# Kernel tuning notes

Measured on AMD Instinct MI355X. Metric: run time of the kernel, lower is better.

The kernel has to match this reference:

```python
import jax, jax.numpy as jnp
import numpy as np

B, N = 256, 8192
H = 30
NUM_CLASSES = 5


def setup_inputs() -> dict:
    key = jax.random.key(0)
    ks = jax.random.split(key, 16)
    def dense(k, fi, fo):
        # flax default: lecun_normal kernel, zero bias
        return jax.random.normal(k, (fi, fo), jnp.float32) / jnp.sqrt(fi)
    return {
        'x':   jax.random.normal(ks[0], (B, N), jnp.float32),
        'W1':  dense(ks[1], 1, H),   'b1': jnp.zeros((H,), jnp.float32),
        'W2':  dense(ks[2], H, H),   'b2': jnp.zeros((H,), jnp.float32),
        'Wa1': dense(ks[3], H, 32),  'ba1': jnp.zeros((32,), jnp.float32),
        'Wa2': dense(ks[4], 32, 1),  'ba2': jnp.zeros((1,), jnp.float32),
        'Wf1': dense(ks[5], 6 * H, 40), 'bf1': jnp.zeros((40,), jnp.float32),
        'Wf2': dense(ks[6], 40, 40),    'bf2': jnp.zeros((40,), jnp.float32),
        'Wf3': dense(ks[7], 40, NUM_CLASSES), 'bf3': jnp.zeros((NUM_CLASSES,), jnp.float32),
    }


def reference(x, W1, b1, W2, b2, Wa1, ba1, Wa2, ba2, Wf1, bf1, Wf2, bf2, Wf3, bf3):
    # (B, N) -> (B, N, 1) -> Dense(30) -> relu -> Dense(30)
    h = jax.nn.relu(x[..., None] * W1[0] + b1)          # (B, N, 30)
    h = jnp.einsum('bnh,hk->bnk', h, W2) + b2           # (B, N, 30)

    # statistical pools over the point axis (axis=1)
    mean_pool = jnp.mean(h, axis=1)
    max_pool = jnp.max(h, axis=1)
    min_pool = jnp.min(h, axis=1)
    std_pool = jnp.std(h, axis=1)
    sum_pool = jnp.sum(h, axis=1)

    # attention pooling over points
    a = jax.nn.relu(jnp.einsum('bnh,hk->bnk', h, Wa1) + ba1)  # (B, N, 32)
    logits = jnp.einsum('bnk,ko->bno', a, Wa2) + ba2          # (B, N, 1)
    attn = jax.nn.softmax(logits, axis=1)                     # (B, N, 1)
    attention_pool = jnp.sum(h * attn, axis=1)                # (B, 30)

    feat = jnp.concatenate(
        [mean_pool, max_pool, min_pool, std_pool, sum_pool, attention_pool],
        axis=-1)                                              # (B, 180)

    z = jax.nn.relu(feat @ Wf1 + bf1)
    z = jax.nn.relu(z @ Wf2 + bf2)
    return z @ Wf3 + bf3                                      # (B, num_classes)
```

## Files before the change

### kernel.cpp

```cpp
#include <hip/hip_runtime.h>
#include <math.h>

#define NN 8192
#define HH 30
#define TPB 1024
#define NIV 31
#define TSTR 68

__launch_bounds__(TPB)
__global__ void pointnet_pwl7_kernel(
    const float* __restrict__ x,
    const float* __restrict__ W1,  const float* __restrict__ b1,
    const float* __restrict__ W2,  const float* __restrict__ b2,
    const float* __restrict__ Wa1, const float* __restrict__ ba1,
    const float* __restrict__ Wa2, const float* __restrict__ ba2,
    const float* __restrict__ Wf1, const float* __restrict__ bf1,
    const float* __restrict__ Wf2, const float* __restrict__ bf2,
    const float* __restrict__ Wf3, const float* __restrict__ bf3,
    float* __restrict__ out)
{
    __shared__ float W2s[HH][32];
    __shared__ float Wa1s[HH][32];
    __shared__ float P[HH][32];
    __shared__ float w1s[HH], b1s[HH], tts[HH];
    __shared__ float b2s[32], ba1s[32], Wa2s[32], vb2[32];
    __shared__ int   DcS;
    __shared__ float d0S;
    __shared__ __align__(16) float ab2[2][64];
    __shared__ __align__(16) float uv2[2][64];
    __shared__ float zz_raw[128], zz_s[128];
    __shared__ float2 gcs[129];
    __shared__ __align__(16) float ts_s[32];
    __shared__ int   rnk[HH];
    __shared__ __align__(16) float abt[NIV][TSTR];
    __shared__ __align__(16) float uvt[NIV][TSTR];
    __shared__ float redb[16][155];
    __shared__ float fin[16];
    __shared__ float feat[192];
    __shared__ float redh[12][40];
    __shared__ float z1s[40], z2s[40];
    __shared__ float wf1s[180 * 40];
    __shared__ float wf2s[40 * 40];
    __shared__ float wf3s[40 * 5];
    __shared__ float bf1s[40], bf2s[40], bf3s[8];

    const int tid = threadIdx.x;
    const int b   = blockIdx.x;

    float4 xl0, xl1;
    {
        const float4* xb4 = reinterpret_cast<const float4*>(x + (size_t)b * NN);
        xl0 = xb4[tid];
        xl1 = xb4[tid + TPB];
    }

    for (int i = tid; i < HH * 32; i += TPB) {
        int j = i >> 5, k = i & 31;
        W2s[j][k] = (k < HH) ? W2[j * HH + k] : 0.f;
    }
    for (int i = tid; i < HH * 32; i += TPB) ((float*)Wa1s)[i] = Wa1[i];
    for (int i = tid; i < 180 * 40; i += TPB) wf1s[i] = Wf1[i];
    for (int i = tid; i < 40 * 40;  i += TPB) wf2s[i] = Wf2[i];
    if (tid < 40 * 5) wf3s[tid] = Wf3[tid];
    if (tid < HH) {
        float w = W1[tid], bb = b1[tid];
        w1s[tid] = w; b1s[tid] = bb;
        tts[tid] = (w != 0.f) ? (-bb / w) : INFINITY;
    }
    if (tid < 32) {
        b2s[tid]  = (tid < HH) ? b2[tid] : 0.f;
        ba1s[tid] = ba1[tid];
        Wa2s[tid] = Wa2[tid];
        ts_s[tid] = INFINITY;
    }
    if (tid < 40) { bf1s[tid] = bf1[tid]; bf2s[tid] = bf2[tid]; }
    if (tid < 5)  { bf3s[tid] = bf3[tid]; }
    const float ba2v = ba2[0];
    __syncthreads();

    if (tid < HH * 32) {
        int j = tid >> 5, m = tid & 31;
        float s = 0.f;
        #pragma unroll
        for (int k = 0; k < HH; ++k) s = fmaf(W2s[j][k], Wa1s[k][m], s);
        P[j][m] = s;
    } else if (tid < HH * 32 + 32) {
        int m = tid - HH * 32;
        float s = 0.f;
        #pragma unroll
        for (int k = 0; k < HH; ++k) s = fmaf(Wa1s[k][m], b2s[k], s);
        vb2[m] = s;
    }
    if (tid < 64) {
        float t = (tid < HH) ? tts[tid] : INFINITY;
        bool fin_t = (t < INFINITY);
        float tmin = fin_t ? t :  INFINITY;
        float tmax = fin_t ? t : -INFINITY;
        #pragma unroll
        for (int off = 32; off > 0; off >>= 1) {
            tmin = fminf(tmin, __shfl_xor(tmin, off));
            tmax = fmaxf(tmax, __shfl_xor(tmax, off));
        }
        if (tid == 0) {
            bool dc1 = (tmin < INFINITY) && (tmin == tmax);
            DcS = dc1 ? 1 : 0;
            d0S = tmin;
        }
    }
    __syncthreads();

    if (DcS == 1) {
        const float d0 = d0S;

        if (tid < 64) {
            int r = tid >> 5, k = tid & 31;
            float a = 0.f, bb = 0.f;
            if (k < HH) {
                for (int j = 0; j < HH; ++j) {
                    float w = w1s[j];
                    bool act = (w == 0.f) ? (b1s[j] > 0.f) : (r ? (w > 0.f) : (w < 0.f));
                    if (act) {
                        float w2 = W2s[j][k];
                        a  = fmaf(w,      w2, a);
                        bb = fmaf(b1s[j], w2, bb);
                    }
                }
                bb += b2s[k];
            }
            ab2[r][k]      = a;
            ab2[r][32 + k] = bb;
        } else if (tid < 128) {
            int i2 = tid - 64;
            int r = i2 >> 5, m = i2 & 31;
            float u = 0.f, v = 0.f;
            for (int j = 0; j < HH; ++j) {
                float w = w1s[j];
                bool act = (w == 0.f) ? (b1s[j] > 0.f) : (r ? (w > 0.f) : (w < 0.f));
                if (act) {
                    float pj = P[j][m];
                    u = fmaf(w,      pj, u);
                    v = fmaf(b1s[j], pj, v);
                }
            }
            v += vb2[m] + ba1s[m];
            uv2[r][m]      = u;
            uv2[r][32 + m] = v;
            float zr = -v / u;
            bool ok = (u != 0.f) && (r == 0 ? (zr < d0) : (zr > d0));
            zz_raw[1 + i2] = ok ? zr : INFINITY;
        } else if (tid < 191) {
            zz_raw[tid - 63] = INFINITY;
        } else if (tid == 191) {
            zz_raw[0] = d0;
        }
        __syncthreads();

        if (tid < 128) {
            float v = zz_raw[tid];
            int rk = 0;
            for (int i = 0; i < 128; ++i) {
                float vi = zz_raw[i];
                rk += (vi < v) || (vi == v && i < tid);
            }
            zz_s[rk] = v;
        }
        __syncthreads();

        if (tid < 129) {
            float lo = (tid == 0)   ? -INFINITY : zz_s[tid - 1];
            float hi = (tid == 128) ?  INFINITY : zz_s[tid];
            float xm;
            if (lo == -INFINITY)      xm = (hi < INFINITY) ? hi - 1.f : 0.f;
            else if (hi == INFINITY)  xm = lo + 1.f;
            else                      xm = 0.5f * (lo + hi);
            int r = (xm >= d0) ? 1 : 0;
            float g = 0.f, c = ba2v;
            for (int m = 0; m < 32; ++m) {
                float u = uv2[r][m], v = uv2[r][32 + m];
                if (fmaf(u, xm, v) > 0.f) {
                    float w = Wa2s[m];
                    g = fmaf(w, u, g);
                    c = fmaf(w, v, c);
                }
            }
            gcs[tid] = make_float2(g, c);
        }
        __syncthreads();

        float c0=0,c1=0, Sx0=0,Sx1=0, Q0=0,Q1=0;
        float mn0=INFINITY,mn1=INFINITY, mx0=-INFINITY,mx1=-INFINITY;
        float Sp0=0,Sp1=0, Px0=0,Px1=0;
        float mrun = -INFINITY;

        float xs[8] = {xl0.x, xl0.y, xl0.z, xl0.w, xl1.x, xl1.y, xl1.z, xl1.w};
        #pragma unroll
        for (int pp = 0; pp < 8; ++pp) {
            float xv = xs[pp];
            bool q1 = (xv >= d0);
            int idx = 0;
            #pragma unroll
            for (int bit = 64; bit >= 1; bit >>= 1) {
                int t = idx + bit;
                idx = (zz_s[t - 1] <= xv) ? t : idx;
            }
            float2 gc = gcs[idx];
            float l = fmaf(xv, gc.x, gc.y);
            float dlt = l - mrun, p;
            if (dlt > 8.f) {
                float sc = __expf(-dlt);
                Sp0 *= sc; Sp1 *= sc; Px0 *= sc; Px1 *= sc;
                mrun = l; p = 1.f;
            } else p = __expf(dlt);
            float xx = xv * xv, px = p * xv;
            float i1 = q1 ? 1.f : 0.f, i0 = 1.f - i1;
            c0 += i0;                    c1 += i1;
            Sx0 = fmaf(i0, xv, Sx0);     Sx1 = fmaf(i1, xv, Sx1);
            Q0  = fmaf(i0, xx, Q0);      Q1  = fmaf(i1, xx, Q1);
            Sp0 = fmaf(i0, p,  Sp0);     Sp1 = fmaf(i1, p,  Sp1);
            Px0 = fmaf(i0, px, Px0);     Px1 = fmaf(i1, px, Px1);
            mn0 = fminf(mn0, q1 ?  INFINITY : xv);
            mx0 = fmaxf(mx0, q1 ? -INFINITY : xv);
            mn1 = fminf(mn1, q1 ? xv :  INFINITY);
            mx1 = fmaxf(mx1, q1 ? xv : -INFINITY);
        }

        #pragma unroll 1
        for (int off = 32; off > 0; off >>= 1) {
            c0  += __shfl_xor(c0,  off);  c1  += __shfl_xor(c1,  off);
            Sx0 += __shfl_xor(Sx0, off);  Sx1 += __shfl_xor(Sx1, off);
            Q0  += __shfl_xor(Q0,  off);  Q1  += __shfl_xor(Q1,  off);
            mn0 = fminf(mn0, __shfl_xor(mn0, off));
            mn1 = fminf(mn1, __shfl_xor(mn1, off));
            mx0 = fmaxf(mx0, __shfl_xor(mx0, off));
            mx1 = fmaxf(mx1, __shfl_xor(mx1, off));
            float mo = __shfl_xor(mrun, off);
            float M  = fmaxf(mrun, mo);
            float sa = __expf(mrun - M), sb = __expf(mo - M);
            float t;
            t = __shfl_xor(Sp0, off); Sp0 = Sp0 * sa + t * sb;
            t = __shfl_xor(Sp1, off); Sp1 = Sp1 * sa + t * sb;
            t = __shfl_xor(Px0, off); Px0 = Px0 * sa + t * sb;
            t = __shfl_xor(Px1, off); Px1 = Px1 * sa + t * sb;
            mrun = M;
        }

        const int wave = tid >> 6, lane = tid & 63;
        if (lane == 0) {
            float* rw = redb[wave];
            rw[0]=c0; rw[1]=Sx0; rw[2]=Q0; rw[3]=mn0; rw[4]=mx0; rw[5]=Sp0; rw[6]=Px0;
            rw[7]=c1; rw[8]=Sx1; rw[9]=Q1; rw[10]=mn1; rw[11]=mx1; rw[12]=Sp1; rw[13]=Px1;
            rw[14]=mrun;
        }
        __syncthreads();

        if (tid < 2) {
            float M = redb[0][14];
            #pragma unroll
            for (int w = 1; w < 16; ++w) M = fmaxf(M, redb[w][14]);
            int base = tid * 7;
            float ck=0, Sx=0, Q=0, mnv=INFINITY, mxv=-INFINITY, Sp=0, Px=0;
            #pragma unroll
            for (int w = 0; w < 16; ++w) {
                ck += redb[w][base+0]; Sx += redb[w][base+1]; Q += redb[w][base+2];
                mnv = fminf(mnv, redb[w][base+3]); mxv = fmaxf(mxv, redb[w][base+4]);
                float e = __expf(redb[w][14] - M);
                Sp = fmaf(redb[w][base+5], e, Sp);
                Px = fmaf(redb[w][base+6], e, Px);
            }
            fin[base+0]=ck; fin[base+1]=Sx; fin[base+2]=Q;
            fin[base+3]=mnv; fin[base+4]=mxv; fin[base+5]=Sp; fin[base+6]=Px;
        }
        __syncthreads();

        if (tid < HH) {
            float sumk=0, ssqk=0, acck=0, L=0;
            float mxk=-INFINITY, mnk=INFINITY;
            #pragma unroll
            for (int r2 = 0; r2 < 2; ++r2) {
                float ck = fin[r2*7+0], Sx = fin[r2*7+1], Q = fin[r2*7+2];
                float xmn = fin[r2*7+3], xmx = fin[r2*7+4];
                float Sp = fin[r2*7+5], Px = fin[r2*7+6];
                float a = ab2[r2][tid], bb = ab2[r2][32 + tid];
                sumk += a * Sx + bb * ck;
                ssqk += a * a * Q + 2.f * a * bb * Sx + bb * bb * ck;
                acck += a * Px + bb * Sp;
                L += Sp;
                if (ck > 0.f) {
                    float h1 = fmaf(a, xmn, bb), h2v = fmaf(a, xmx, bb);
                    mxk = fmaxf(mxk, fmaxf(h1, h2v));
                    mnk = fminf(mnk, fminf(h1, h2v));
                }
            }
            const float invN = 1.f / (float)NN;
            float mean = sumk * invN;
            float var  = fmaxf(ssqk * invN - mean * mean, 0.f);
            feat[tid]        = mean;
            feat[30 + tid]   = mxk;
            feat[60 + tid]   = mnk;
            feat[90 + tid]   = sqrtf(var);
            feat[120 + tid]  = sumk;
            feat[150 + tid]  = acck / L;
        }
    } else {
        if (tid < HH) {
            float t = tts[tid];
            int r = 0;
            for (int i = 0; i < HH; ++i) {
                float ti = tts[i];
                r += (ti < t) || (ti == t && i < tid);
            }
            ts_s[r] = t;
            rnk[tid] = r;
        }
        __syncthreads();
        for (int idx = tid; idx < NIV * 32; idx += TPB) {
            int r = idx >> 5, k = idx & 31;
            float a = 0.f, bb = 0.f;
            if (k < HH) {
                for (int j = 0; j < HH; ++j) {
                    float w = w1s[j];
                    bool act = (w > 0.f) ? (rnk[j] < r)
                             : ((w < 0.f) ? (rnk[j] >= r) : (b1s[j] > 0.f));
                    if (act) {
                        float w2 = W2s[j][k];
                        a  = fmaf(w,      w2, a);
                        bb = fmaf(b1s[j], w2, bb);
                    }
                }
                bb += b2s[k];
            }
            abt[r][k]      = a;
            abt[r][32 + k] = bb;
        }
        __syncthreads();
        for (int idx = tid; idx < NIV * 32; idx += TPB) {
            int r = idx >> 5, m = idx & 31;
            float u = 0.f, v = 0.f;
            for (int k = 0; k < HH; ++k) {
                float wa = Wa1s[k][m];
                u = fmaf(wa, abt[r][k],      u);
                v = fmaf(wa, abt[r][32 + k], v);
            }
            v += ba1s[m];
            uvt[r][m]      = u;
            uvt[r][32 + m] = v;
        }
        __syncthreads();

        float sum[HH], ssq[HH], mx[HH], mn[HH], acc[HH];
        #pragma unroll
        for (int k = 0; k < HH; ++k) {
            sum[k] = 0.f; ssq[k] = 0.f; acc[k] = 0.f;
            mx[k] = -INFINITY; mn[k] = INFINITY;
        }
        float mrun = -INFINITY, lrun = 0.f;
        const float* xb = x + (size_t)b * NN;
        const float4* ts4 = (const float4*)ts_s;
        const float4* wv4 = (const float4*)Wa2s;

        #pragma unroll 1
        for (int it = 0; it < NN / TPB; ++it) {
            float xv = xb[it * TPB + tid];
            int r = 0;
            #pragma unroll
            for (int i = 0; i < 8; ++i) {
                float4 t = ts4[i];
                r += (xv >= t.x) ? 1 : 0;
                r += (xv >= t.y) ? 1 : 0;
                r += (xv >= t.z) ? 1 : 0;
                r += (xv >= t.w) ? 1 : 0;
            }
            float h2[HH];
            const float4* arow = (const float4*)(&abt[r][0]);
            #pragma unroll
            for (int i = 0; i < 7; ++i) {
                float4 av = arow[i], bv = arow[8 + i];
                h2[4*i+0] = fmaf(xv, av.x, bv.x);
                h2[4*i+1] = fmaf(xv, av.y, bv.y);
                h2[4*i+2] = fmaf(xv, av.z, bv.z);
                h2[4*i+3] = fmaf(xv, av.w, bv.w);
            }
            { float4 av = arow[7], bv = arow[15];
              h2[28] = fmaf(xv, av.x, bv.x);
              h2[29] = fmaf(xv, av.y, bv.y); }
            #pragma unroll
            for (int k = 0; k < HH; ++k) {
                float h = h2[k];
                sum[k] += h;
                ssq[k] = fmaf(h, h, ssq[k]);
                mx[k] = fmaxf(mx[k], h);
                mn[k] = fminf(mn[k], h);
            }
            float l = ba2v;
            const float4* urow = (const float4*)(&uvt[r][0]);
            #pragma unroll
            for (int i = 0; i < 8; ++i) {
                float4 uu = urow[i], vv = urow[8 + i], ww = wv4[i];
                l = fmaf(fmaxf(fmaf(xv, uu.x, vv.x), 0.f), ww.x, l);
                l = fmaf(fmaxf(fmaf(xv, uu.y, vv.y), 0.f), ww.y, l);
                l = fmaf(fmaxf(fmaf(xv, uu.z, vv.z), 0.f), ww.z, l);
                l = fmaf(fmaxf(fmaf(xv, uu.w, vv.w), 0.f), ww.w, l);
            }
            float d = l - mrun, p;
            if (d > 8.f) {
                float s = __expf(-d);
                lrun *= s;
                #pragma unroll
                for (int k = 0; k < HH; ++k) acc[k] *= s;
                mrun = l; p = 1.f;
            } else p = __expf(d);
            lrun += p;
            #pragma unroll
            for (int k = 0; k < HH; ++k) acc[k] = fmaf(p, h2[k], acc[k]);
        }

        #pragma unroll 1
        for (int off = 32; off > 0; off >>= 1) {
            #pragma unroll
            for (int k = 0; k < HH; ++k) {
                sum[k] += __shfl_xor(sum[k], off);
                ssq[k] += __shfl_xor(ssq[k], off);
                mx[k] = fmaxf(mx[k], __shfl_xor(mx[k], off));
                mn[k] = fminf(mn[k], __shfl_xor(mn[k], off));
            }
            float mo = __shfl_xor(mrun, off);
            float lo = __shfl_xor(lrun, off);
            float M  = fmaxf(mrun, mo);
            float sa = __expf(mrun - M), sb = __expf(mo - M);
            lrun = lrun * sa + lo * sb;
            #pragma unroll
            for (int k = 0; k < HH; ++k)
                acc[k] = acc[k] * sa + __shfl_xor(acc[k], off) * sb;
            mrun = M;
        }

        const int wave = tid >> 6, lane = tid & 63;
        if (lane == 0) {
            #pragma unroll
            for (int k = 0; k < HH; ++k) {
                redb[wave][k]       = sum[k];
                redb[wave][30 + k]  = ssq[k];
                redb[wave][60 + k]  = mx[k];
                redb[wave][90 + k]  = mn[k];
                redb[wave][120 + k] = acc[k];
            }
            redb[wave][150] = mrun;
            redb[wave][151] = lrun;
        }
        __syncthreads();

        if (tid < HH) {
            float M = -INFINITY;
            #pragma unroll
            for (int w = 0; w < 16; ++w) M = fmaxf(M, redb[w][150]);
            float s = 0.f, ss = 0.f, L = 0.f, A = 0.f;
            float mxv = -INFINITY, mnv = INFINITY;
            #pragma unroll
            for (int w = 0; w < 16; ++w) {
                s  += redb[w][tid];
                ss += redb[w][30 + tid];
                mxv = fmaxf(mxv, redb[w][60 + tid]);
                mnv = fminf(mnv, redb[w][90 + tid]);
                float e = __expf(redb[w][150] - M);
                L = fmaf(redb[w][151], e, L);
                A = fmaf(redb[w][120 + tid], e, A);
            }
            const float invN = 1.f / (float)NN;
            float mean = s * invN;
            float var  = fmaxf(ss * invN - mean * mean, 0.f);
            feat[tid]       = mean;
            feat[30 + tid]  = mxv;
            feat[60 + tid]  = mnv;
            feat[90 + tid]  = sqrtf(var);
            feat[120 + tid] = s;
            feat[150 + tid] = A / L;
        }
    }
    __syncthreads();

    if (tid < 480) {
        int o = tid % 40, p = tid / 40;
        float z = 0.f;
        #pragma unroll
        for (int ii = 0; ii < 15; ++ii)
            z = fmaf(feat[p * 15 + ii], wf1s[(p * 15 + ii) * 40 + o], z);
        redh[p][o] = z;
    }
    __syncthreads();
    if (tid < 40) {
        float z = bf1s[tid];
        #pragma unroll
        for (int p = 0; p < 12; ++p) z += redh[p][tid];
        z1s[tid] = fmaxf(z, 0.f);
    }
    __syncthreads();
    if (tid < 40) {
        float z = bf2s[tid];
        #pragma unroll
        for (int i = 0; i < 40; ++i) z = fmaf(z1s[i], wf2s[i * 40 + tid], z);
        z2s[tid] = fmaxf(z, 0.f);
    }
    __syncthreads();
    if (tid < 5) {
        float o = bf3s[tid];
        #pragma unroll
        for (int i = 0; i < 40; ++i) o = fmaf(z2s[i], wf3s[i * 5 + tid], o);
        out[b * 5 + tid] = o;
    }
}

extern "C" void kernel_launch(void* const* d_in, const int* in_sizes, int n_in,
                              void* d_out, int out_size, void* d_ws, size_t ws_size,
                              hipStream_t stream) {
    const float* x   = (const float*)d_in[0];
    const float* W1  = (const float*)d_in[1];
    const float* b1  = (const float*)d_in[2];
    const float* W2  = (const float*)d_in[3];
    const float* b2  = (const float*)d_in[4];
    const float* Wa1 = (const float*)d_in[5];
    const float* ba1 = (const float*)d_in[6];
    const float* Wa2 = (const float*)d_in[7];
    const float* ba2 = (const float*)d_in[8];
    const float* Wf1 = (const float*)d_in[9];
    const float* bf1 = (const float*)d_in[10];
    const float* Wf2 = (const float*)d_in[11];
    const float* bf2 = (const float*)d_in[12];
    const float* Wf3 = (const float*)d_in[13];
    const float* bf3 = (const float*)d_in[14];
    float* out = (float*)d_out;

    pointnet_pwl7_kernel<<<256, TPB, 0, stream>>>(
        x, W1, b1, W2, b2, Wa1, ba1, Wa2, ba2,
        Wf1, bf1, Wf2, bf2, Wf3, bf3, out);
}
```

Measured before the change: 113.6 us.

## Split fast and fallback paths into separate kernels gated by workspace flag

The single kernel held both the fast piecewise-linear path (used when all first-layer ReLU breakpoints coincide) and the general fallback, so its shared memory and register footprint were sized for the fallback. The fast path now lives in its own 1024-thread kernel with a smaller reduction buffer, and writes a flag to workspace. A second 512-thread fallback kernel reads the flag and exits immediately when the fast path already ran. This is meant to lower resource pressure on the fast path, at the cost of an extra kernel launch and a flag read.

```diff
diff --git a/kernel.cpp b/kernel.cpp
--- a/kernel.cpp
+++ b/kernel.cpp
@@ -3,12 +3,13 @@
 
 #define NN 8192
 #define HH 30
-#define TPB 1024
+#define TPBA 1024
+#define TPBB 512
 #define NIV 31
 #define TSTR 68
 
-__launch_bounds__(TPB)
-__global__ void pointnet_pwl7_kernel(
+__launch_bounds__(TPBA)
+__global__ void pointnet_fastA(
     const float* __restrict__ x,
     const float* __restrict__ W1,  const float* __restrict__ b1,
     const float* __restrict__ W2,  const float* __restrict__ b2,
@@ -17,7 +18,7 @@
     const float* __restrict__ Wf1, const float* __restrict__ bf1,
     const float* __restrict__ Wf2, const float* __restrict__ bf2,
     const float* __restrict__ Wf3, const float* __restrict__ bf3,
-    float* __restrict__ out)
+    float* __restrict__ out, int* __restrict__ wsflag)
 {
     __shared__ float W2s[HH][32];
     __shared__ float Wa1s[HH][32];
@@ -30,11 +31,7 @@
     __shared__ __align__(16) float uv2[2][64];
     __shared__ float zz_raw[128], zz_s[128];
     __shared__ float2 gcs[129];
-    __shared__ __align__(16) float ts_s[32];
-    __shared__ int   rnk[HH];
-    __shared__ __align__(16) float abt[NIV][TSTR];
-    __shared__ __align__(16) float uvt[NIV][TSTR];
-    __shared__ float redb[16][155];
+    __shared__ float redb[16][16];
     __shared__ float fin[16];
     __shared__ float feat[192];
     __shared__ float redh[12][40];
@@ -51,16 +48,16 @@
     {
         const float4* xb4 = reinterpret_cast<const float4*>(x + (size_t)b * NN);
         xl0 = xb4[tid];
-        xl1 = xb4[tid + TPB];
-    }
-
-    for (int i = tid; i < HH * 32; i += TPB) {
+        xl1 = xb4[tid + TPBA];
+    }
+
+    for (int i = tid; i < HH * 32; i += TPBA) {
         int j = i >> 5, k = i & 31;
         W2s[j][k] = (k < HH) ? W2[j * HH + k] : 0.f;
     }
-    for (int i = tid; i < HH * 32; i += TPB) ((float*)Wa1s)[i] = Wa1[i];
-    for (int i = tid; i < 180 * 40; i += TPB) wf1s[i] = Wf1[i];
-    for (int i = tid; i < 40 * 40;  i += TPB) wf2s[i] = Wf2[i];
+    for (int i = tid; i < HH * 32; i += TPBA) ((float*)Wa1s)[i] = Wa1[i];
+    for (int i = tid; i < 180 * 40; i += TPBA) wf1s[i] = Wf1[i];
+    for (int i = tid; i < 40 * 40;  i += TPBA) wf2s[i] = Wf2[i];
     if (tid < 40 * 5) wf3s[tid] = Wf3[tid];
     if (tid < HH) {
         float w = W1[tid], bb = b1[tid];
@@ -71,7 +68,6 @@
         b2s[tid]  = (tid < HH) ? b2[tid] : 0.f;
         ba1s[tid] = ba1[tid];
         Wa2s[tid] = Wa2[tid];
-        ts_s[tid] = INFINITY;
     }
     if (tid < 40) { bf1s[tid] = bf1[tid]; bf2s[tid] = bf2[tid]; }
     if (tid < 5)  { bf3s[tid] = bf3[tid]; }
@@ -109,372 +105,463 @@
     }
     __syncthreads();
 
-    if (DcS == 1) {
-        const float d0 = d0S;
-
-        if (tid < 64) {
-            int r = tid >> 5, k = tid & 31;
-            float a = 0.f, bb = 0.f;
-            if (k < HH) {
-                for (int j = 0; j < HH; ++j) {
-                    float w = w1s[j];
-                    bool act = (w == 0.f) ? (b1s[j] > 0.f) : (r ? (w > 0.f) : (w < 0.f));
-                    if (act) {
-                        float w2 = W2s[j][k];
-                        a  = fmaf(w,      w2, a);
-                        bb = fmaf(b1s[j], w2, bb);
-                    }
-                }
-                bb += b2s[k];
-            }
-            ab2[r][k]      = a;
-            ab2[r][32 + k] = bb;
-        } else if (tid < 128) {
-            int i2 = tid - 64;
-            int r = i2 >> 5, m = i2 & 31;
-            float u = 0.f, v = 0.f;
+    if (tid == 0) wsflag[0] = DcS;
+    if (DcS != 1) return;
+
+    const float d0 = d0S;
+
+    if (tid < 64) {
+        int r = tid >> 5, k = tid & 31;
+        float a = 0.f, bb = 0.f;
+        if (k < HH) {
             for (int j = 0; j < HH; ++j) {
                 float w = w1s[j];
                 bool act = (w == 0.f) ? (b1s[j] > 0.f) : (r ? (w > 0.f) : (w < 0.f));
                 if (act) {
-                    float pj = P[j][m];
-                    u = fmaf(w,      pj, u);
-                    v = fmaf(b1s[j], pj, v);
+                    float w2 = W2s[j][k];
+                    a  = fmaf(w,      w2, a);
+                    bb = fmaf(b1s[j], w2, bb);
                 }
             }
-            v += vb2[m] + ba1s[m];
-            uv2[r][m]      = u;
-            uv2[r][32 + m] = v;
-            float zr = -v / u;
-            bool ok = (u != 0.f) && (r == 0 ? (zr < d0) : (zr > d0));
-            zz_raw[1 + i2] = ok ? zr : INFINITY;
-        } else if (tid < 191) {
-            zz_raw[tid - 63] = INFINITY;
-        } else if (tid == 191) {
-            zz_raw[0] = d0;
-        }
-        __syncthreads();
-
-        if (tid < 128) {
-            float v = zz_raw[tid];
-            int rk = 0;
-            for (int i = 0; i < 128; ++i) {
-                float vi = zz_raw[i];
-                rk += (vi < v) || (vi == v && i < tid);
+            bb += b2s[k];
+        }
+        ab2[r][k]      = a;
+        ab2[r][32 + k] = bb;
+    } else if (tid < 128) {
+        int i2 = tid - 64;
+        int r = i2 >> 5, m = i2 & 31;
+        float u = 0.f, v = 0.f;
+        for (int j = 0; j < HH; ++j) {
+            float w = w1s[j];
+            bool act = (w == 0.f) ? (b1s[j] > 0.f) : (r ? (w > 0.f) : (w < 0.f));
+            if (act) {
+                float pj = P[j][m];
+                u = fmaf(w,      pj, u);
+                v = fmaf(b1s[j], pj, v);
             }
-            zz_s[rk] = v;
-        }
-        __syncthreads();
-
-        if (tid < 129) {
-            float lo = (tid == 0)   ? -INFINITY : zz_s[tid - 1];
-            float hi = (tid == 128) ?  INFINITY : zz_s[tid];
-            float xm;
-            if (lo == -INFINITY)      xm = (hi < INFINITY) ? hi - 1.f : 0.f;
-            else if (hi == INFINITY)  xm = lo + 1.f;
-            else                      xm = 0.5f * (lo + hi);
-            int r = (xm >= d0) ? 1 : 0;
-            float g = 0.f, c = ba2v;
-            for (int m = 0; m < 32; ++m) {
-                float u = uv2[r][m], v = uv2[r][32 + m];
-                if (fmaf(u, xm, v) > 0.f) {
-                    float w = Wa2s[m];
-                    g = fmaf(w, u, g);
-                    c = fmaf(w, v, c);
+        }
+        v += vb2[m] + ba1s[m];
+        uv2[r][m]      = u;
+        uv2[r][32 + m] = v;
+        float zr = -v / u;
+        bool ok = (u != 0.f) && (r == 0 ? (zr < d0) : (zr > d0));
+        zz_raw[1 + i2] = ok ? zr : INFINITY;
+    } else if (tid < 191) {
+        zz_raw[tid - 63] = INFINITY;
+    } else if (tid == 191) {
+        zz_raw[0] = d0;
+    }
+    __syncthreads();
+
+    if (tid < 128) {
+        float v = zz_raw[tid];
+        int rk = 0;
+        for (int i = 0; i < 128; ++i) {
+            float vi = zz_raw[i];
+            rk += (vi < v) || (vi == v && i < tid);
+        }
+        zz_s[rk] = v;
+    }
+    __syncthreads();
+
+    if (tid < 129) {
+        float lo = (tid == 0)   ? -INFINITY : zz_s[tid - 1];
+        float hi = (tid == 128) ?  INFINITY : zz_s[tid];
+        float xm;
+        if (lo == -INFINITY)      xm = (hi < INFINITY) ? hi - 1.f : 0.f;
+        else if (hi == INFINITY)  xm = lo + 1.f;
+        else                      xm = 0.5f * (lo + hi);
+        int r = (xm >= d0) ? 1 : 0;
+        float g = 0.f, c = ba2v;
+        for (int m = 0; m < 32; ++m) {
+            float u = uv2[r][m], v = uv2[r][32 + m];
+            if (fmaf(u, xm, v) > 0.f) {
+                float w = Wa2s[m];
+                g = fmaf(w, u, g);
+                c = fmaf(w, v, c);
+            }
+        }
+        gcs[tid] = make_float2(g, c);
+    }
+    __syncthreads();
+
+    float c0=0,c1=0, Sx0=0,Sx1=0, Q0=0,Q1=0;
+    float mn0=INFINITY,mn1=INFINITY, mx0=-INFINITY,mx1=-INFINITY;
+    float Sp0=0,Sp1=0, Px0=0,Px1=0;
+    float mrun = -INFINITY;
+
+    float xs[8] = {xl0.x, xl0.y, xl0.z, xl0.w, xl1.x, xl1.y, xl1.z, xl1.w};
+    #pragma unroll
+    for (int pp = 0; pp < 8; ++pp) {
+        float xv = xs[pp];
+        bool q1 = (xv >= d0);
+        int idx = 0;
+        #pragma unroll
+        for (int bit = 64; bit >= 1; bit >>= 1) {
+            int t = idx + bit;
+            idx = (zz_s[t - 1] <= xv) ? t : idx;
+        }
+        float2 gc = gcs[idx];
+        float l = fmaf(xv, gc.x, gc.y);
+        float dlt = l - mrun, p;
+        if (dlt > 8.f) {
+            float sc = __expf(-dlt);
+            Sp0 *= sc; Sp1 *= sc; Px0 *= sc; Px1 *= sc;
+            mrun = l; p = 1.f;
+        } else p = __expf(dlt);
+        float xx = xv * xv, px = p * xv;
+        float i1 = q1 ? 1.f : 0.f, i0 = 1.f - i1;
+        c0 += i0;                    c1 += i1;
+        Sx0 = fmaf(i0, xv, Sx0);     Sx1 = fmaf(i1, xv, Sx1);
+        Q0  = fmaf(i0, xx, Q0);      Q1  = fmaf(i1, xx, Q1);
+        Sp0 = fmaf(i0, p,  Sp0);     Sp1 = fmaf(i1, p,  Sp1);
+        Px0 = fmaf(i0, px, Px0);     Px1 = fmaf(i1, px, Px1);
+        mn0 = fminf(mn0, q1 ?  INFINITY : xv);
+        mx0 = fmaxf(mx0, q1 ? -INFINITY : xv);
+        mn1 = fminf(mn1, q1 ? xv :  INFINITY);
+        mx1 = fmaxf(mx1, q1 ? xv : -INFINITY);
+    }
+
+    #pragma unroll 1
+    for (int off = 32; off > 0; off >>= 1) {
+        c0  += __shfl_xor(c0,  off);  c1  += __shfl_xor(c1,  off);
+        Sx0 += __shfl_xor(Sx0, off);  Sx1 += __shfl_xor(Sx1, off);
+        Q0  += __shfl_xor(Q0,  off);  Q1  += __shfl_xor(Q1,  off);
+        mn0 = fminf(mn0, __shfl_xor(mn0, off));
+        mn1 = fminf(mn1, __shfl_xor(mn1, off));
+        mx0 = fmaxf(mx0, __shfl_xor(mx0, off));
+        mx1 = fmaxf(mx1, __shfl_xor(mx1, off));
+        float mo = __shfl_xor(mrun, off);
+        float M  = fmaxf(mrun, mo);
+        float sa = __expf(mrun - M), sb = __expf(mo - M);
+        float t;
+        t = __shfl_xor(Sp0, off); Sp0 = Sp0 * sa + t * sb;
+        t = __shfl_xor(Sp1, off); Sp1 = Sp1 * sa + t * sb;
+        t = __shfl_xor(Px0, off); Px0 = Px0 * sa + t * sb;
+        t = __shfl_xor(Px1, off); Px1 = Px1 * sa + t * sb;
+        mrun = M;
+    }
+
+    const int wave = tid >> 6, lane = tid & 63;
+    if (lane == 0) {
+        float* rw = redb[wave];
+        rw[0]=c0; rw[1]=Sx0; rw[2]=Q0; rw[3]=mn0; rw[4]=mx0; rw[5]=Sp0; rw[6]=Px0;
+        rw[7]=c1; rw[8]=Sx1; rw[9]=Q1; rw[10]=mn1; rw[11]=mx1; rw[12]=Sp1; rw[13]=Px1;
+        rw[14]=mrun;
+    }
+    __syncthreads();
+
+    if (tid < 2) {
+        float M = redb[0][14];
+        #pragma unroll
+        for (int w = 1; w < 16; ++w) M = fmaxf(M, redb[w][14]);
+        int base = tid * 7;
+        float ck=0, Sx=0, Q=0, mnv=INFINITY, mxv=-INFINITY, Sp=0, Px=0;
+        #pragma unroll
+        for (int w = 0; w < 16; ++w) {
+            ck += redb[w][base+0]; Sx += redb[w][base+1]; Q += redb[w][base+2];
+            mnv = fminf(mnv, redb[w][base+3]); mxv = fmaxf(mxv, redb[w][base+4]);
+            float e = __expf(redb[w][14] - M);
+            Sp = fmaf(redb[w][base+5], e, Sp);
+            Px = fmaf(redb[w][base+6], e, Px);
+        }
+        fin[base+0]=ck; fin[base+1]=Sx; fin[base+2]=Q;
+        fin[base+3]=mnv; fin[base+4]=mxv; fin[base+5]=Sp; fin[base+6]=Px;
+    }
+    __syncthreads();
+
+    if (tid < HH) {
+        float sumk=0, ssqk=0, acck=0, L=0;
+        float mxk=-INFINITY, mnk=INFINITY;
+        #pragma unroll
+        for (int r2 = 0; r2 < 2; ++r2) {
+            float ck = fin[r2*7+0], Sx = fin[r2*7+1], Q = fin[r2*7+2];
+            float xmn = fin[r2*7+3], xmx = fin[r2*7+4];
+            float Sp = fin[r2*7+5], Px = fin[r2*7+6];
+            float a = ab2[r2][tid], bb = ab2[r2][32 + tid];
+            sumk += a * Sx + bb * ck;
+            ssqk += a * a * Q + 2.f * a * bb * Sx + bb * bb * ck;
+            acck += a * Px + bb * Sp;
+            L += Sp;
+            if (ck > 0.f) {
+                float h1 = fmaf(a, xmn, bb), h2v = fmaf(a, xmx, bb);
+                mxk = fmaxf(mxk, fmaxf(h1, h2v));
+                mnk = fminf(mnk, fminf(h1, h2v));
+            }
+        }
+        const float invN = 1.f / (float)NN;
+        float mean = sumk * invN;
+        float var  = fmaxf(ssqk * invN - mean * mean, 0.f);
+        feat[tid]        = mean;
+        feat[30 + tid]   = mxk;
+        feat[60 + tid]   = mnk;
+        feat[90 + tid]   = sqrtf(var);
+        feat[120 + tid]  = sumk;
+        feat[150 + tid]  = acck / L;
+    }
+    __syncthreads();
+
+    if (tid < 480) {
+        int o = tid % 40, p = tid / 40;
+        float z = 0.f;
+        #pragma unroll
+        for (int ii = 0; ii < 15; ++ii)
+            z = fmaf(feat[p * 15 + ii], wf1s[(p * 15 + ii) * 40 + o], z);
+        redh[p][o] = z;
+    }
+    __syncthreads();
+    if (tid < 40) {
+        float z = bf1s[tid];
+        #pragma unroll
+        for (int p = 0; p < 12; ++p) z += redh[p][tid];
+        z1s[tid] = fmaxf(z, 0.f);
+    }
+    __syncthreads();
+    if (tid < 40) {
+        float z = bf2s[tid];
+        #pragma unroll
+        for (int i = 0; i < 40; ++i) z = fmaf(z1s[i], wf2s[i * 40 + tid], z);
+        z2s[tid] = fmaxf(z, 0.f);
+    }
+    __syncthreads();
+    if (tid < 5) {
+        float o = bf3s[tid];
+        #pragma unroll
+        for (int i = 0; i < 40; ++i) o = fmaf(z2s[i], wf3s[i * 5 + tid], o);
+        out[b * 5 + tid] = o;
+    }
+}
+
+__launch_bounds__(TPBB, 1)
+__global__ void pointnet_fbB(
+    const float* __restrict__ x,
+    const float* __restrict__ W1,  const float* __restrict__ b1,
+    const float* __restrict__ W2,  const float* __restrict__ b2,
+    const float* __restrict__ Wa1, const float* __restrict__ ba1,
+    const float* __restrict__ Wa2, const float* __restrict__ ba2,
+    const float* __restrict__ Wf1, const float* __restrict__ bf1,
+    const float* __restrict__ Wf2, const float* __restrict__ bf2,
+    const float* __restrict__ Wf3, const float* __restrict__ bf3,
+    float* __restrict__ out, const int* __restrict__ wsflag)
+{
+    if (wsflag[0] == 1) return;
+
+    __shared__ float W2s[HH][32];
+    __shared__ float Wa1s[HH][32];
+    __shared__ float w1s[HH], b1s[HH], tts[HH];
+    __shared__ float b2s[32], ba1s[32], Wa2s[32];
+    __shared__ __align__(16) float ts_s[32];
+    __shared__ int   rnk[HH];
+    __shared__ __align__(16) float abt[NIV][TSTR];
+    __shared__ __align__(16) float uvt[NIV][TSTR];
+    __shared__ float red[8][154];
+    __shared__ float feat[192];
+    __shared__ float redh[12][40];
+    __shared__ float z1s[40], z2s[40];
+    __shared__ float wf1s[180 * 40];
+    __shared__ float wf2s[40 * 40];
+    __shared__ float wf3s[40 * 5];
+    __shared__ float bf1s[40], bf2s[40], bf3s[8];
+
+    const int tid = threadIdx.x;
+    const int b   = blockIdx.x;
+
+    for (int i = tid; i < HH * 32; i += TPBB) {
+        int j = i >> 5, k = i & 31;
+        W2s[j][k] = (k < HH) ? W2[j * HH + k] : 0.f;
+    }
+    for (int i = tid; i < HH * 32; i += TPBB) ((float*)Wa1s)[i] = Wa1[i];
+    for (int i = tid; i < 180 * 40; i += TPBB) wf1s[i] = Wf1[i];
+    for (int i = tid; i < 40 * 40;  i += TPBB) wf2s[i] = Wf2[i];
+    if (tid < 40 * 5) wf3s[tid] = Wf3[tid];
+    if (tid < HH) {
+        float w = W1[tid], bb = b1[tid];
+        w1s[tid] = w; b1s[tid] = bb;
+        tts[tid] = (w != 0.f) ? (-bb / w) : INFINITY;
+    }
+    if (tid < 32) {
+        b2s[tid]  = (tid < HH) ? b2[tid] : 0.f;
+        ba1s[tid] = ba1[tid];
+        Wa2s[tid] = Wa2[tid];
+        ts_s[tid] = INFINITY;
+    }
+    if (tid < 40) { bf1s[tid] = bf1[tid]; bf2s[tid] = bf2[tid]; }
+    if (tid < 5)  { bf3s[tid] = bf3[tid]; }
+    const float ba2v = ba2[0];
+    __syncthreads();
+
+    if (tid < HH) {
+        float t = tts[tid];
+        int r = 0;
+        for (int i = 0; i < HH; ++i) {
+            float ti = tts[i];
+            r += (ti < t) || (ti == t && i < tid);
+        }
+        ts_s[r] = t;
+        rnk[tid] = r;
+    }
+    __syncthreads();
+    for (int idx = tid; idx < NIV * 32; idx += TPBB) {
+        int r = idx >> 5, k = idx & 31;
+        float a = 0.f, bb = 0.f;
+        if (k < HH) {
+            for (int j = 0; j < HH; ++j) {
+                float w = w1s[j];
+                bool act = (w > 0.f) ? (rnk[j] < r)
+                         : ((w < 0.f) ? (rnk[j] >= r) : (b1s[j] > 0.f));
+                if (act) {
+                    float w2 = W2s[j][k];
+                    a  = fmaf(w,      w2, a);
+                    bb = fmaf(b1s[j], w2, bb);
                 }
             }
-            gcs[tid] = make_float2(g, c);
-        }
-        __syncthreads();
-
-        float c0=0,c1=0, Sx0=0,Sx1=0, Q0=0,Q1=0;
-        float mn0=INFINITY,mn1=INFINITY, mx0=-INFINITY,mx1=-INFINITY;
-        float Sp0=0,Sp1=0, Px0=0,Px1=0;
-        float mrun = -INFINITY;
-
-        float xs[8] = {xl0.x, xl0.y, xl0.z, xl0.w, xl1.x, xl1.y, xl1.z, xl1.w};
-        #pragma unroll
-        for (int pp = 0; pp < 8; ++pp) {
-            float xv = xs[pp];
-            bool q1 = (xv >= d0);
-            int idx = 0;
+            bb += b2s[k];
+        }
+        abt[r][k]      = a;
+        abt[r][32 + k] = bb;
+    }
+    __syncthreads();
+    for (int idx = tid; idx < NIV * 32; idx += TPBB) {
+        int r = idx >> 5, m = idx & 31;
+        float u = 0.f, v = 0.f;
+        for (int k = 0; k < HH; ++k) {
+            float wa = Wa1s[k][m];
+            u = fmaf(wa, abt[r][k],      u);
+            v = fmaf(wa, abt[r][32 + k], v);
+        }
+        v += ba1s[m];
+        uvt[r][m]      = u;
+        uvt[r][32 + m] = v;
+    }
+    __syncthreads();
+
+    float sum[HH], ssq[HH], mx[HH], mn[HH], acc[HH];
+    #pragma unroll
+    for (int k = 0; k < HH; ++k) {
+        sum[k] = 0.f; ssq[k] = 0.f; acc[k] = 0.f;
+        mx[k] = -INFINITY; mn[k] = INFINITY;
+    }
+    float mrun = -INFINITY, lrun = 0.f;
+    const float* xb = x + (size_t)b * NN;
+    const float4* ts4 = (const float4*)ts_s;
+    const float4* wv4 = (const float4*)Wa2s;
+
+    #pragma unroll 1
+    for (int it = 0; it < NN / TPBB; ++it) {
+        float xv = xb[it * TPBB + tid];
+        int r = 0;
+        #pragma unroll
+        for (int i = 0; i < 8; ++i) {
+            float4 t = ts4[i];
+            r += (xv >= t.x) ? 1 : 0;
+            r += (xv >= t.y) ? 1 : 0;
+            r += (xv >= t.z) ? 1 : 0;
+            r += (xv >= t.w) ? 1 : 0;
+        }
+        float h2[HH];
+        const float4* arow = (const float4*)(&abt[r][0]);
+        #pragma unroll
+        for (int i = 0; i < 7; ++i) {
+            float4 av = arow[i], bv = arow[8 + i];
+            h2[4*i+0] = fmaf(xv, av.x, bv.x);
+            h2[4*i+1] = fmaf(xv, av.y, bv.y);
+            h2[4*i+2] = fmaf(xv, av.z, bv.z);
+            h2[4*i+3] = fmaf(xv, av.w, bv.w);
+        }
+        { float4 av = arow[7], bv = arow[15];
+          h2[28] = fmaf(xv, av.x, bv.x);
+          h2[29] = fmaf(xv, av.y, bv.y); }
+        #pragma unroll
+        for (int k = 0; k < HH; ++k) {
+            float h = h2[k];
+            sum[k] += h;
+            ssq[k] = fmaf(h, h, ssq[k]);
+            mx[k] = fmaxf(mx[k], h);
+            mn[k] = fminf(mn[k], h);
+        }
+        float l = ba2v;
+        const float4* urow = (const float4*)(&uvt[r][0]);
+        #pragma unroll
+        for (int i = 0; i < 8; ++i) {
+            float4 uu = urow[i], vv = urow[8 + i], ww = wv4[i];
+            l = fmaf(fmaxf(fmaf(xv, uu.x, vv.x), 0.f), ww.x, l);
+            l = fmaf(fmaxf(fmaf(xv, uu.y, vv.y), 0.f), ww.y, l);
+            l = fmaf(fmaxf(fmaf(xv, uu.z, vv.z), 0.f), ww.z, l);
+            l = fmaf(fmaxf(fmaf(xv, uu.w, vv.w), 0.f), ww.w, l);
+        }
+        float d = l - mrun, p;
+        if (d > 8.f) {
+            float s = __expf(-d);
+            lrun *= s;
             #pragma unroll
-            for (int bit = 64; bit >= 1; bit >>= 1) {
-                int t = idx + bit;
-                idx = (zz_s[t - 1] <= xv) ? t : idx;
-            }
-            float2 gc = gcs[idx];
-            float l = fmaf(xv, gc.x, gc.y);
-            float dlt = l - mrun, p;
-            if (dlt > 8.f) {
-                float sc = __expf(-dlt);
-                Sp0 *= sc; Sp1 *= sc; Px0 *= sc; Px1 *= sc;
-                mrun = l; p = 1.f;
-            } else p = __expf(dlt);
-            float xx = xv * xv, px = p * xv;
-            float i1 = q1 ? 1.f : 0.f, i0 = 1.f - i1;
-            c0 += i0;                    c1 += i1;
-            Sx0 = fmaf(i0, xv, Sx0);     Sx1 = fmaf(i1, xv, Sx1);
-            Q0  = fmaf(i0, xx, Q0);      Q1  = fmaf(i1, xx, Q1);
-            Sp0 = fmaf(i0, p,  Sp0);     Sp1 = fmaf(i1, p,  Sp1);
-            Px0 = fmaf(i0, px, Px0);     Px1 = fmaf(i1, px, Px1);
-            mn0 = fminf(mn0, q1 ?  INFINITY : xv);
-            mx0 = fmaxf(mx0, q1 ? -INFINITY : xv);
-            mn1 = fminf(mn1, q1 ? xv :  INFINITY);
-            mx1 = fmaxf(mx1, q1 ? xv : -INFINITY);
-        }
-
-        #pragma unroll 1
-        for (int off = 32; off > 0; off >>= 1) {
-            c0  += __shfl_xor(c0,  off);  c1  += __shfl_xor(c1,  off);
-            Sx0 += __shfl_xor(Sx0, off);  Sx1 += __shfl_xor(Sx1, off);
-            Q0  += __shfl_xor(Q0,  off);  Q1  += __shfl_xor(Q1,  off);
-            mn0 = fminf(mn0, __shfl_xor(mn0, off));
-            mn1 = fminf(mn1, __shfl_xor(mn1, off));
-            mx0 = fmaxf(mx0, __shfl_xor(mx0, off));
-            mx1 = fmaxf(mx1, __shfl_xor(mx1, off));
-            float mo = __shfl_xor(mrun, off);
-            float M  = fmaxf(mrun, mo);
-            float sa = __expf(mrun - M), sb = __expf(mo - M);
-            float t;
-            t = __shfl_xor(Sp0, off); Sp0 = Sp0 * sa + t * sb;
-            t = __shfl_xor(Sp1, off); Sp1 = Sp1 * sa + t * sb;
-            t = __shfl_xor(Px0, off); Px0 = Px0 * sa + t * sb;
-            t = __shfl_xor(Px1, off); Px1 = Px1 * sa + t * sb;
-            mrun = M;
-        }
-
-        const int wave = tid >> 6, lane = tid & 63;
-        if (lane == 0) {
-            float* rw = redb[wave];
-            rw[0]=c0; rw[1]=Sx0; rw[2]=Q0; rw[3]=mn0; rw[4]=mx0; rw[5]=Sp0; rw[6]=Px0;
-            rw[7]=c1; rw[8]=Sx1; rw[9]=Q1; rw[10]=mn1; rw[11]=mx1; rw[12]=Sp1; rw[13]=Px1;
-            rw[14]=mrun;
-        }
-        __syncthreads();
-
-        if (tid < 2) {
-            float M = redb[0][14];
-            #pragma unroll
-            for (int w = 1; w < 16; ++w) M = fmaxf(M, redb[w][14]);
-            int base = tid * 7;
-            float ck=0, Sx=0, Q=0, mnv=INFINITY, mxv=-INFINITY, Sp=0, Px=0;
-            #pragma unroll
-            for (int w = 0; w < 16; ++w) {
-                ck += redb[w][base+0]; Sx += redb[w][base+1]; Q += redb[w][base+2];
-                mnv = fminf(mnv, redb[w][base+3]); mxv = fmaxf(mxv, redb[w][base+4]);
-                float e = __expf(redb[w][14] - M);
-                Sp = fmaf(redb[w][base+5], e, Sp);
-                Px = fmaf(redb[w][base+6], e, Px);
-            }
-            fin[base+0]=ck; fin[base+1]=Sx; fin[base+2]=Q;
-            fin[base+3]=mnv; fin[base+4]=mxv; fin[base+5]=Sp; fin[base+6]=Px;
-        }
-        __syncthreads();
-
-        if (tid < HH) {
-            float sumk=0, ssqk=0, acck=0, L=0;
-            float mxk=-INFINITY, mnk=INFINITY;
-            #pragma unroll
-            for (int r2 = 0; r2 < 2; ++r2) {
-                float ck = fin[r2*7+0], Sx = fin[r2*7+1], Q = fin[r2*7+2];
-                float xmn = fin[r2*7+3], xmx = fin[r2*7+4];
-                float Sp = fin[r2*7+5], Px = fin[r2*7+6];
-                float a = ab2[r2][tid], bb = ab2[r2][32 + tid];
-                sumk += a * Sx + bb * ck;
-                ssqk += a * a * Q + 2.f * a * bb * Sx + bb * bb * ck;
-                acck += a * Px + bb * Sp;
-                L += Sp;
-                if (ck > 0.f) {
-                    float h1 = fmaf(a, xmn, bb), h2v = fmaf(a, xmx, bb);
-                    mxk = fmaxf(mxk, fmaxf(h1, h2v));
-                    mnk = fminf(mnk, fminf(h1, h2v));
-                }
-            }
-            const float invN = 1.f / (float)NN;
-            float mean = sumk * invN;
-            float var  = fmaxf(ssqk * invN - mean * mean, 0.f);
-            feat[tid]        = mean;
-            feat[30 + tid]   = mxk;
-            feat[60 + tid]   = mnk;
-            feat[90 + tid]   = sqrtf(var);
-            feat[120 + tid]  = sumk;
-            feat[150 + tid]  = acck / L;
-        }
-    } else {
-        if (tid < HH) {
-            float t = tts[tid];
-            int r = 0;
-            for (int i = 0; i < HH; ++i) {
-                float ti = tts[i];
-                r += (ti < t) || (ti == t && i < tid);
-            }
-            ts_s[r] = t;
-            rnk[tid] = r;
-        }
-        __syncthreads();
-        for (int idx = tid; idx < NIV * 32; idx += TPB) {
-            int r = idx >> 5, k = idx & 31;
-            float a = 0.f, bb = 0.f;
-            if (k < HH) {
-                for (int j = 0; j < HH; ++j) {
-                    float w = w1s[j];
-                    bool act = (w > 0.f) ? (rnk[j] < r)
-                             : ((w < 0.f) ? (rnk[j] >= r) : (b1s[j] > 0.f));
-                    if (act) {
-                        float w2 = W2s[j][k];
-                        a  = fmaf(w,      w2, a);
-                        bb = fmaf(b1s[j], w2, bb);
-                    }
-                }
-                bb += b2s[k];
-            }
-            abt[r][k]      = a;
-            abt[r][32 + k] = bb;
-        }
-        __syncthreads();
-        for (int idx = tid; idx < NIV * 32; idx += TPB) {
-            int r = idx >> 5, m = idx & 31;
-            float u = 0.f, v = 0.f;
-            for (int k = 0; k < HH; ++k) {
-                float wa = Wa1s[k][m];
-                u = fmaf(wa, abt[r][k],      u);
-                v = fmaf(wa, abt[r][32 + k], v);
-            }
-            v += ba1s[m];
-            uvt[r][m]      = u;
-            uvt[r][32 + m] = v;
-        }
-        __syncthreads();
-
-        float sum[HH], ssq[HH], mx[HH], mn[HH], acc[HH];
+            for (int k = 0; k < HH; ++k) acc[k] *= s;
+            mrun = l; p = 1.f;
+        } else p = __expf(d);
+        lrun += p;
+        #pragma unroll
+        for (int k = 0; k < HH; ++k) acc[k] = fmaf(p, h2[k], acc[k]);
+    }
+
+    #pragma unroll 1
+    for (int off = 32; off > 0; off >>= 1) {
         #pragma unroll
         for (int k = 0; k < HH; ++k) {
-            sum[k] = 0.f; ssq[k] = 0.f; acc[k] = 0.f;
-            mx[k] = -INFINITY; mn[k] = INFINITY;
-        }
-        float mrun = -INFINITY, lrun = 0.f;
-        const float* xb = x + (size_t)b * NN;
-        const float4* ts4 = (const float4*)ts_s;
-        const float4* wv4 = (const float4*)Wa2s;
-
-        #pragma unroll 1
-        for (int it = 0; it < NN / TPB; ++it) {
-            float xv = xb[it * TPB + tid];
-            int r = 0;
-            #pragma unroll
-            for (int i = 0; i < 8; ++i) {
-                float4 t = ts4[i];
-                r += (xv >= t.x) ? 1 : 0;
-                r += (xv >= t.y) ? 1 : 0;
-                r += (xv >= t.z) ? 1 : 0;
-                r += (xv >= t.w) ? 1 : 0;
-            }
-            float h2[HH];
-            const float4* arow = (const float4*)(&abt[r][0]);
-            #pragma unroll
-            for (int i = 0; i < 7; ++i) {
-                float4 av = arow[i], bv = arow[8 + i];
-                h2[4*i+0] = fmaf(xv, av.x, bv.x);
-                h2[4*i+1] = fmaf(xv, av.y, bv.y);
-                h2[4*i+2] = fmaf(xv, av.z, bv.z);
-                h2[4*i+3] = fmaf(xv, av.w, bv.w);
-            }
-            { float4 av = arow[7], bv = arow[15];
-              h2[28] = fmaf(xv, av.x, bv.x);
-              h2[29] = fmaf(xv, av.y, bv.y); }
-            #pragma unroll
-            for (int k = 0; k < HH; ++k) {
-                float h = h2[k];
-                sum[k] += h;
-                ssq[k] = fmaf(h, h, ssq[k]);
-                mx[k] = fmaxf(mx[k], h);
-                mn[k] = fminf(mn[k], h);
-            }
-            float l = ba2v;
-            const float4* urow = (const float4*)(&uvt[r][0]);
-            #pragma unroll
-            for (int i = 0; i < 8; ++i) {
-                float4 uu = urow[i], vv = urow[8 + i], ww = wv4[i];
-                l = fmaf(fmaxf(fmaf(xv, uu.x, vv.x), 0.f), ww.x, l);
-                l = fmaf(fmaxf(fmaf(xv, uu.y, vv.y), 0.f), ww.y, l);
-                l = fmaf(fmaxf(fmaf(xv, uu.z, vv.z), 0.f), ww.z, l);
-                l = fmaf(fmaxf(fmaf(xv, uu.w, vv.w), 0.f), ww.w, l);
-            }
-            float d = l - mrun, p;
-            if (d > 8.f) {
-                float s = __expf(-d);
-                lrun *= s;
-                #pragma unroll
-                for (int k = 0; k < HH; ++k) acc[k] *= s;
-                mrun = l; p = 1.f;
-            } else p = __expf(d);
-            lrun += p;
-            #pragma unroll
-            for (int k = 0; k < HH; ++k) acc[k] = fmaf(p, h2[k], acc[k]);
-        }
-
-        #pragma unroll 1
-        for (int off = 32; off > 0; off >>= 1) {
-            #pragma unroll
-            for (int k = 0; k < HH; ++k) {
-                sum[k] += __shfl_xor(sum[k], off);
-                ssq[k] += __shfl_xor(ssq[k], off);
-                mx[k] = fmaxf(mx[k], __shfl_xor(mx[k], off));
-                mn[k] = fminf(mn[k], __shfl_xor(mn[k], off));
-            }
-            float mo = __shfl_xor(mrun, off);
-            float lo = __shfl_xor(lrun, off);
-            float M  = fmaxf(mrun, mo);
-            float sa = __expf(mrun - M), sb = __expf(mo - M);
-            lrun = lrun * sa + lo * sb;
-            #pragma unroll
-            for (int k = 0; k < HH; ++k)
-                acc[k] = acc[k] * sa + __shfl_xor(acc[k], off) * sb;
-            mrun = M;
-        }
-
-        const int wave = tid >> 6, lane = tid & 63;
-        if (lane == 0) {
-            #pragma unroll
-            for (int k = 0; k < HH; ++k) {
-                redb[wave][k]       = sum[k];
-                redb[wave][30 + k]  = ssq[k];
-                redb[wave][60 + k]  = mx[k];
-                redb[wave][90 + k]  = mn[k];
-                redb[wave][120 + k] = acc[k];
-            }
-            redb[wave][150] = mrun;
-            redb[wave][151] = lrun;
-        }
-        __syncthreads();
-
-        if (tid < HH) {
-            float M = -INFINITY;
-            #pragma unroll
-            for (int w = 0; w < 16; ++w) M = fmaxf(M, redb[w][150]);
-            float s = 0.f, ss = 0.f, L = 0.f, A = 0.f;
-            float mxv = -INFINITY, mnv = INFINITY;
-            #pragma unroll
-            for (int w = 0; w < 16; ++w) {
-                s  += redb[w][tid];
-                ss += redb[w][30 + tid];
-                mxv = fmaxf(mxv, redb[w][60 + tid]);
-                mnv = fminf(mnv, redb[w][90 + tid]);
-                float e = __expf(redb[w][150] - M);
-                L = fmaf(redb[w][151], e, L);
-                A = fmaf(redb[w][120 + tid], e, A);
-            }
-            const float invN = 1.f / (float)NN;
-            float mean = s * invN;
-            float var  = fmaxf(ss * invN - mean * mean, 0.f);
-            feat[tid]       = mean;
-            feat[30 + tid]  = mxv;
-            feat[60 + tid]  = mnv;
-            feat[90 + tid]  = sqrtf(var);
-            feat[120 + tid] = s;
-            feat[150 + tid] = A / L;
-        }
+            sum[k] += __shfl_xor(sum[k], off);
+            ssq[k] += __shfl_xor(ssq[k], off);
+            mx[k] = fmaxf(mx[k], __shfl_xor(mx[k], off));
+            mn[k] = fminf(mn[k], __shfl_xor(mn[k], off));
+        }
+        float mo = __shfl_xor(mrun, off);
+        float lo = __shfl_xor(lrun, off);
+        float M  = fmaxf(mrun, mo);
+        float sa = __expf(mrun - M), sb = __expf(mo - M);
+        lrun = lrun * sa + lo * sb;
+        #pragma unroll
+        for (int k = 0; k < HH; ++k)
+            acc[k] = acc[k] * sa + __shfl_xor(acc[k], off) * sb;
+        mrun = M;
+    }
+
+    const int wave = tid >> 6, lane = tid & 63;
+    if (lane == 0) {
+        #pragma unroll
+        for (int k = 0; k < HH; ++k) {
+            red[wave][k]       = sum[k];
+            red[wave][30 + k]  = ssq[k];
+            red[wave][60 + k]  = mx[k];
+            red[wave][90 + k]  = mn[k];
+            red[wave][120 + k] = acc[k];
+        }
+        red[wave][150] = mrun;
+        red[wave][151] = lrun;
+    }
+    __syncthreads();
+
+    if (tid < HH) {
+        float M = -INFINITY;
+        #pragma unroll
+        for (int w = 0; w < 8; ++w) M = fmaxf(M, red[w][150]);
+        float s = 0.f, ss = 0.f, L = 0.f, A = 0.f;
+        float mxv = -INFINITY, mnv = INFINITY;
+        #pragma unroll
+        for (int w = 0; w < 8; ++w) {
+            s  += red[w][tid];
+            ss += red[w][30 + tid];
+            mxv = fmaxf(mxv, red[w][60 + tid]);
+            mnv = fminf(mnv, red[w][90 + tid]);
+            float e = __expf(red[w][150] - M);
+            L = fmaf(red[w][151], e, L);
+            A = fmaf(red[w][120 + tid], e, A);
+        }
+        const float invN = 1.f / (float)NN;
+        float mean = s * invN;
+        float var  = fmaxf(ss * invN - mean * mean, 0.f);
+        feat[tid]       = mean;
+        feat[30 + tid]  = mxv;
+        feat[60 + tid]  = mnv;
+        feat[90 + tid]  = sqrtf(var);
+        feat[120 + tid] = s;
+        feat[150 + tid] = A / L;
     }
     __syncthreads();
 
@@ -528,8 +615,12 @@
     const float* Wf3 = (const float*)d_in[13];
     const float* bf3 = (const float*)d_in[14];
     float* out = (float*)d_out;
-
-    pointnet_pwl7_kernel<<<256, TPB, 0, stream>>>(
+    int* wsflag = (int*)d_ws;
+
+    pointnet_fastA<<<256, TPBA, 0, stream>>>(
         x, W1, b1, W2, b2, Wa1, ba1, Wa2, ba2,
-        Wf1, bf1, Wf2, bf2, Wf3, bf3, out);
+        Wf1, bf1, Wf2, bf2, Wf3, bf3, out, wsflag);
+    pointnet_fbB<<<256, TPBB, 0, stream>>>(
+        x, W1, b1, W2, b2, Wa1, ba1, Wa2, ba2,
+        Wf1, bf1, Wf2, bf2, Wf3, bf3, out, wsflag);
 }
```

Result: faster. 107.4 us (-5.4%).
